# Kernel optimization log

Hardware: AMD Instinct MI355X
Metric: run time of the kernel (lower is better)

The kernel has to match this reference:

```python
import jax, jax.numpy as jnp
import numpy as np

B, C, H, W = 16, 1024, 32, 32
M = 32

def setup_inputs() -> dict:
    key = jax.random.key(0)
    k1, k2 = jax.random.split(key)
    features = jax.random.normal(k1, (B, C, H, W), dtype=jnp.float32)
    raw_attentions = jax.random.normal(k2, (B, M, H, W), dtype=jnp.float32)
    return {"features": features, "raw_attentions": raw_attentions}

def reference(features, raw_attentions):
    # non_lin='sigmoid'
    attentions = jax.nn.sigmoid(raw_attentions)  # [B, M, H, W]
    # GAP pooling of features * attentions[:, i] for each map i, fused as one
    # contraction: feature_matrix[b, m, c] = mean_{h,w} features[b,c,h,w] * att[b,m,h,w]
    hw = features.shape[2] * features.shape[3]
    feature_matrix = jnp.einsum('bchw,bmhw->bmc', features, attentions) / hw  # [B, M, C]
    return feature_matrix, attentions
```

## Files before the change

### kernel.cpp

```cpp
#include <hip/hip_runtime.h>
#include <cstdint>
#include <cstddef>


#define BB 16
#define CC 1024
#define MM 32
#define HW 1024

#define TCR 32
#define TKF 128
#define NSTF (HW / TKF)
#define ND 4

typedef __attribute__((ext_vector_type(4))) float f32x4;
typedef __attribute__((ext_vector_type(8))) float f32x8;
typedef __attribute__((ext_vector_type(8))) short s16x8;

__device__ inline short bf16rne(float x)
{
    uint32_t u = __builtin_bit_cast(uint32_t, x);
    u = (u + 0x7FFFu + ((u >> 16) & 1u)) >> 16;
    return (short)u;
}

__device__ inline s16x8 cvt8(f32x4 lo, f32x4 hi)
{
    s16x8 r;
#pragma unroll
    for (int j = 0; j < 4; ++j) {
        r[j]     = bf16rne(lo[j]);
        r[4 + j] = bf16rne(hi[j]);
    }
    return r;
}

__device__ inline void gld_lds16(const void* g, void* l)
{
    __builtin_amdgcn_global_load_lds(
        (const __attribute__((address_space(1))) void*)g,
        (__attribute__((address_space(3))) void*)l, 16, 0, 0);
}

__global__ __launch_bounds__(256) void sigmoid_kernel(
    const float* __restrict__ raw, float* __restrict__ out1,
    unsigned short* __restrict__ ws)
{
    int g = blockIdx.x * 256 + threadIdx.x;
    f32x8 v = reinterpret_cast<const f32x8*>(raw)[g];
    f32x8 s;
    s16x8 h;
#pragma unroll
    for (int j = 0; j < 8; ++j) {
        s[j] = 1.0f / (1.0f + __expf(-v[j]));
        h[j] = bf16rne(s[j]);
    }
    reinterpret_cast<f32x8*>(out1)[g] = s;
    reinterpret_cast<s16x8*>(ws)[g] = h;
}

__global__ __launch_bounds__(256) void bap_mfma(
    const float* __restrict__ feat,
    const unsigned short* __restrict__ ws,
    float* __restrict__ out0)
{
    __shared__ float fsh[ND][TCR][TKF];

    const int t  = threadIdx.x;
    const int w  = t >> 6;
    const int l  = t & 63;
    const int b  = blockIdx.x & 15;
    const int ct = blockIdx.x >> 4;
    const int cbase = ct * TCR;

    const int lrow  = l >> 5;
    const int lslot = l & 31;

    const float* fbase = feat + (size_t)(b * CC + cbase) * HW;

    auto stage = [&](int s) {
        const int nb = s & (ND - 1);
        const int k0 = s * TKF;
#pragma unroll
        for (int i = 0; i < 4; ++i) {
            int r0  = w * 8 + i * 2;
            int row = r0 + lrow;
            int sg  = lslot ^ (row & 15);
            gld_lds16(fbase + (size_t)row * HW + k0 + sg * 4,
                      &fsh[nb][r0][0]);
        }
    };

    const int r  = l & 15;
    const int q  = l >> 4;
    const int mt = w >> 1;
    const int c2 = w & 1;
    const int arow = mt * 16 + r;
    const int brow = c2 * 16 + r;
    const s16x8* ap = reinterpret_cast<const s16x8*>(
        ws + (size_t)(b * MM + arow) * HW);

    s16x8 af[ND][4];
    auto load_af = [&](int s) {
        const int pb = s & (ND - 1);
#pragma unroll
        for (int ch = 0; ch < 4; ++ch) {
            const s16x8* a = ap + s * 16 + ch * 4 + q;
            asm volatile("global_load_dwordx4 %0, %1, off"
                         : "=&v"(af[pb][ch]) : "v"(a) : "memory");
        }
    };

    f32x4 acc = {0.f, 0.f, 0.f, 0.f};

    auto compute = [&](int s) {
        const int nb = s & (ND - 1);
#pragma unroll
        for (int ch = 0; ch < 4; ++ch) {
            const int S0 = ch * 8 + 2 * q;
            f32x4 blo = *reinterpret_cast<const f32x4*>(
                &fsh[nb][brow][(S0 ^ r) * 4]);
            f32x4 bhi = *reinterpret_cast<const f32x4*>(
                &fsh[nb][brow][((S0 + 1) ^ r) * 4]);
            acc = __builtin_amdgcn_mfma_f32_16x16x32_bf16(
                      af[nb][ch], cvt8(blo, bhi), acc, 0, 0, 0);
        }
    };

    load_af(0); stage(0);
    load_af(1); stage(1);
    load_af(2); stage(2);

#pragma unroll
    for (int s = 0; s < NSTF; ++s) {
        const int rem = NSTF - 1 - s;
        if (rem >= 2)      asm volatile("s_waitcnt vmcnt(16)" ::: "memory");
        else if (rem == 1) asm volatile("s_waitcnt vmcnt(8)"  ::: "memory");
        else               asm volatile("s_waitcnt vmcnt(0)"  ::: "memory");
        __builtin_amdgcn_sched_barrier(0);
        __builtin_amdgcn_s_barrier();
        if (s + 3 < NSTF) { load_af(s + 3); stage(s + 3); }
        compute(s);
    }

    const float sc = 1.0f / (float)HW;
    float* p = out0 + (size_t)(b * MM) * CC + cbase + c2 * 16;
#pragma unroll
    for (int reg = 0; reg < 4; ++reg)
        p[(size_t)(mt * 16 + 4 * q + reg) * CC + r] = acc[reg] * sc;
}

extern "C" void kernel_launch(void* const* d_in, const int* in_sizes, int n_in,
                              void* d_out, int out_size, void* d_ws, size_t ws_size,
                              hipStream_t stream)
{
    const float* feat = (const float*)d_in[0];
    const float* raw  = (const float*)d_in[1];
    float* out0 = (float*)d_out;
    float* out1 = out0 + (size_t)BB * MM * HW;
    unsigned short* att_bf = (unsigned short*)d_ws;

    sigmoid_kernel<<<256, 256, 0, stream>>>(raw, out1, att_bf);
    bap_mfma<<<512, 256, 0, stream>>>(feat, att_bf, out0);
}
```

Baseline: 22.66 us.

## Fuse sigmoid into the MFMA pooling kernel, dropping the separate launch

Removes the standalone sigmoid kernel and its bf16 workspace. The GEMM kernel now loads raw fp32 attention values, applies sigmoid and bf16 conversion in registers just before each MFMA, and each block writes one row of the sigmoid output. The attention prefetch depth drops to two stages and the wait counts are retuned to match. This saves a kernel launch and a workspace round trip, at the cost of twice the attention load bytes and sigmoid work repeated across the 32 channel tiles.

```diff
diff --git a/kernel.cpp b/kernel.cpp
--- a/kernel.cpp
+++ b/kernel.cpp
@@ -14,7 +14,6 @@
 #define ND 4
 
 typedef __attribute__((ext_vector_type(4))) float f32x4;
-typedef __attribute__((ext_vector_type(8))) float f32x8;
 typedef __attribute__((ext_vector_type(8))) short s16x8;
 
 __device__ inline short bf16rne(float x)
@@ -35,6 +34,15 @@
     return r;
 }
 
+__device__ inline f32x4 sig4(f32x4 v)
+{
+    f32x4 o;
+#pragma unroll
+    for (int j = 0; j < 4; ++j)
+        o[j] = 1.0f / (1.0f + __expf(-v[j]));
+    return o;
+}
+
 __device__ inline void gld_lds16(const void* g, void* l)
 {
     __builtin_amdgcn_global_load_lds(
@@ -42,27 +50,11 @@
         (__attribute__((address_space(3))) void*)l, 16, 0, 0);
 }
 
-__global__ __launch_bounds__(256) void sigmoid_kernel(
-    const float* __restrict__ raw, float* __restrict__ out1,
-    unsigned short* __restrict__ ws)
-{
-    int g = blockIdx.x * 256 + threadIdx.x;
-    f32x8 v = reinterpret_cast<const f32x8*>(raw)[g];
-    f32x8 s;
-    s16x8 h;
-#pragma unroll
-    for (int j = 0; j < 8; ++j) {
-        s[j] = 1.0f / (1.0f + __expf(-v[j]));
-        h[j] = bf16rne(s[j]);
-    }
-    reinterpret_cast<f32x8*>(out1)[g] = s;
-    reinterpret_cast<s16x8*>(ws)[g] = h;
-}
-
-__global__ __launch_bounds__(256) void bap_mfma(
+__global__ __launch_bounds__(256) void bap_fused(
     const float* __restrict__ feat,
-    const unsigned short* __restrict__ ws,
-    float* __restrict__ out0)
+    const float* __restrict__ raw,
+    float* __restrict__ out0,
+    float* __restrict__ out1)
 {
     __shared__ float fsh[ND][TCR][TKF];
 
@@ -97,17 +89,18 @@
     const int c2 = w & 1;
     const int arow = mt * 16 + r;
     const int brow = c2 * 16 + r;
-    const s16x8* ap = reinterpret_cast<const s16x8*>(
-        ws + (size_t)(b * MM + arow) * HW);
+    const float* ap_raw = raw + (size_t)(b * MM + arow) * HW;
 
-    s16x8 af[ND][4];
+    f32x4 afl[2][4], afh[2][4];
     auto load_af = [&](int s) {
-        const int pb = s & (ND - 1);
+        const int pb = s & 1;
 #pragma unroll
         for (int ch = 0; ch < 4; ++ch) {
-            const s16x8* a = ap + s * 16 + ch * 4 + q;
+            const float* a = ap_raw + s * TKF + ch * 32 + q * 8;
             asm volatile("global_load_dwordx4 %0, %1, off"
-                         : "=&v"(af[pb][ch]) : "v"(a) : "memory");
+                         : "=&v"(afl[pb][ch]) : "v"(a) : "memory");
+            asm volatile("global_load_dwordx4 %0, %1, off offset:16"
+                         : "=&v"(afh[pb][ch]) : "v"(a) : "memory");
         }
     };
 
@@ -115,6 +108,7 @@
 
     auto compute = [&](int s) {
         const int nb = s & (ND - 1);
+        const int pb = s & 1;
 #pragma unroll
         for (int ch = 0; ch < 4; ++ch) {
             const int S0 = ch * 8 + 2 * q;
@@ -122,25 +116,33 @@
                 &fsh[nb][brow][(S0 ^ r) * 4]);
             f32x4 bhi = *reinterpret_cast<const f32x4*>(
                 &fsh[nb][brow][((S0 + 1) ^ r) * 4]);
+            s16x8 af = cvt8(sig4(afl[pb][ch]), sig4(afh[pb][ch]));
             acc = __builtin_amdgcn_mfma_f32_16x16x32_bf16(
-                      af[nb][ch], cvt8(blo, bhi), acc, 0, 0, 0);
+                      af, cvt8(blo, bhi), acc, 0, 0, 0);
         }
     };
 
     load_af(0); stage(0);
     load_af(1); stage(1);
-    load_af(2); stage(2);
+    stage(2);
 
 #pragma unroll
     for (int s = 0; s < NSTF; ++s) {
-        const int rem = NSTF - 1 - s;
-        if (rem >= 2)      asm volatile("s_waitcnt vmcnt(16)" ::: "memory");
-        else if (rem == 1) asm volatile("s_waitcnt vmcnt(8)"  ::: "memory");
-        else               asm volatile("s_waitcnt vmcnt(0)"  ::: "memory");
+        if (s <= 5)      asm volatile("s_waitcnt vmcnt(16)" ::: "memory");
+        else if (s == 6) asm volatile("s_waitcnt vmcnt(12)" ::: "memory");
+        else             asm volatile("s_waitcnt vmcnt(0)"  ::: "memory");
         __builtin_amdgcn_sched_barrier(0);
         __builtin_amdgcn_s_barrier();
-        if (s + 3 < NSTF) { load_af(s + 3); stage(s + 3); }
         compute(s);
+        if (s + 2 < NSTF) load_af(s + 2);
+        if (s + 3 < NSTF) stage(s + 3);
+    }
+
+    {
+        const float* rrow = raw  + (size_t)(b * MM + ct) * HW;
+        float*       orow = out1 + (size_t)(b * MM + ct) * HW;
+        f32x4 rv = reinterpret_cast<const f32x4*>(rrow)[t];
+        reinterpret_cast<f32x4*>(orow)[t] = sig4(rv);
     }
 
     const float sc = 1.0f / (float)HW;
@@ -158,8 +160,6 @@
     const float* raw  = (const float*)d_in[1];
     float* out0 = (float*)d_out;
     float* out1 = out0 + (size_t)BB * MM * HW;
-    unsigned short* att_bf = (unsigned short*)d_ws;
 
-    sigmoid_kernel<<<256, 256, 0, stream>>>(raw, out1, att_bf);
-    bap_mfma<<<512, 256, 0, stream>>>(feat, att_bf, out0);
+    bap_fused<<<512, 256, 0, stream>>>(feat, raw, out0, out1);
 }
```

Result: slower. 31.33 us (+38.3%).
